# Kernel tuning notes

Hardware: AMD Instinct MI355X
Metric: run time of the kernel (lower is better)

The kernel has to match this reference:

```python
import jax, jax.numpy as jnp
import numpy as np
from jax import lax

B, C_IN, IMG, P = 8, 320, 64, 2
H = W = IMG // P            # 32
N = H * W                   # 1024 tokens
DIM = 128 * P * P           # 512
DEPTH, HEADS, DH = 6, 8, 64
INNER = HEADS * DH          # 512
MLP = 512
EPS = 1e-5


def layernorm(x, g, b):
    mu = x.mean(-1, keepdims=True)
    var = ((x - mu) ** 2).mean(-1, keepdims=True)
    return (x - mu) * lax.rsqrt(var + EPS) * g + b


def conv3x3(x, w, b):
    y = lax.conv_general_dilated(x, w, (1, 1), 'SAME',
                                 dimension_numbers=('NCHW', 'OIHW', 'NCHW'))
    return y + b[None, :, None, None]


def posemb_sincos_2d(h, w, dim, temperature=10000.0):
    y, x = jnp.meshgrid(jnp.arange(h, dtype=jnp.float32),
                        jnp.arange(w, dtype=jnp.float32), indexing='ij')
    omega = jnp.arange(dim // 4, dtype=jnp.float32) / (dim // 4 - 1)
    omega = 1.0 / (temperature ** omega)
    y = y.reshape(-1)[:, None] * omega[None, :]
    x = x.reshape(-1)[:, None] * omega[None, :]
    return jnp.concatenate([jnp.sin(x), jnp.cos(x), jnp.sin(y), jnp.cos(y)], axis=1)


def prepare_attn_mask(mask):
    # attn mask allows position pairs where either row or col token is marked.
    f = 64 // H
    m = (mask == 1)
    r = m.reshape(-1, H, f, W, f).any(axis=(2, 4)).reshape(-1, N)  # [M, N] bool
    return r[:, :, None] | r[:, None, :]                            # [M, N, N]


def setup_inputs() -> dict:
    key = jax.random.key(0)
    ks = jax.random.split(key, 24)
    s = 0.02
    d = dict(
        img=jax.random.normal(ks[0], (B, C_IN, IMG, IMG), jnp.float32),
        mask=jax.random.randint(ks[1], (DEPTH * B, 64, 64), 0, 2, jnp.int32),
        conv1_w=jax.random.normal(ks[2], (128, C_IN, 3, 3), jnp.float32) * s,
        conv1_b=jnp.zeros((128,), jnp.float32),
        ln_p_g=jnp.ones((DIM,), jnp.float32), ln_p_b=jnp.zeros((DIM,), jnp.float32),
        proj_w=jax.random.normal(ks[3], (DIM, DIM), jnp.float32) * s,
        proj_b=jnp.zeros((DIM,), jnp.float32),
        ln_q_g=jnp.ones((DIM,), jnp.float32), ln_q_b=jnp.zeros((DIM,), jnp.float32),
        attn_ln_g=jnp.ones((DEPTH, DIM), jnp.float32),
        attn_ln_b=jnp.zeros((DEPTH, DIM), jnp.float32),
        wqkv=jax.random.normal(ks[4], (DEPTH, DIM, 3 * INNER), jnp.float32) * s,
        wo=jax.random.normal(ks[5], (DEPTH, INNER, DIM), jnp.float32) * s,
        ff_ln_g=jnp.ones((DEPTH, DIM), jnp.float32),
        ff_ln_b=jnp.zeros((DEPTH, DIM), jnp.float32),
        w1=jax.random.normal(ks[6], (DEPTH, DIM, MLP), jnp.float32) * s,
        b1=jnp.zeros((DEPTH, MLP), jnp.float32),
        w2=jax.random.normal(ks[7], (DEPTH, MLP, DIM), jnp.float32) * s,
        b2=jnp.zeros((DEPTH, DIM), jnp.float32),
        conv2_w=jax.random.normal(ks[8], (C_IN, 128, 3, 3), jnp.float32) * s,
        conv2_b=jnp.zeros((C_IN,), jnp.float32),
    )
    return d


def reference(img, mask, conv1_w, conv1_b, ln_p_g, ln_p_b, proj_w, proj_b,
              ln_q_g, ln_q_b, attn_ln_g, attn_ln_b, wqkv, wo,
              ff_ln_g, ff_ln_b, w1, b1, w2, b2, conv2_w, conv2_b):
    am = prepare_attn_mask(mask).reshape(DEPTH, B, N, N)  # per-layer masks

    # patch embed: conv -> rearrange 'b c (h p1) (w p2) -> b (h w) (p1 p2 c)'
    y = conv3x3(img, conv1_w, conv1_b)                           # [B,128,64,64]
    y = y.reshape(B, 128, H, P, W, P).transpose(0, 2, 4, 3, 5, 1)
    y = y.reshape(B, N, P * P * 128)                             # [B,N,512]
    x = layernorm(y, ln_p_g, ln_p_b) @ proj_w + proj_b
    x = layernorm(x, ln_q_g, ln_q_b)
    x = x + posemb_sincos_2d(H, W, DIM).astype(x.dtype)

    scale = DH ** -0.5
    for i in range(DEPTH):
        xn = layernorm(x, attn_ln_g[i], attn_ln_b[i])
        qkv = xn @ wqkv[i]                                       # [B,N,3*INNER]
        q, k, v = jnp.split(qkv, 3, axis=-1)
        q, k, v = (t.reshape(B, N, HEADS, DH).transpose(0, 2, 1, 3)
                   for t in (q, k, v))
        dots = jnp.einsum('bhid,bhjd->bhij', q, k) * scale
        min_val = lax.stop_gradient(dots.min())
        dots = jnp.where(am[i][:, None, :, :], dots, min_val)
        attn = jax.nn.softmax(dots, axis=-1)
        o = jnp.einsum('bhij,bhjd->bhid', attn, v)
        o = o.transpose(0, 2, 1, 3).reshape(B, N, INNER) @ wo[i]
        x = o + x
        h = layernorm(x, ff_ln_g[i], ff_ln_b[i]) @ w1[i] + b1[i]
        x = jax.nn.gelu(h, approximate=False) @ w2[i] + b2[i] + x

    # 'b (h w) (p1 p2 c) -> b c (h p1) (w p2)' then conv
    z = x.reshape(B, H, W, P, P, 128).transpose(0, 5, 1, 3, 2, 4)
    z = z.reshape(B, 128, IMG, IMG)
    return conv3x3(z, conv2_w, conv2_b)
```

## Files before the change

kernel.cpp:

```cpp
#include <hip/hip_runtime.h>
#include <hip/hip_bf16.h>
#include <math.h>

typedef __attribute__((ext_vector_type(8))) short short8;
typedef __attribute__((ext_vector_type(4))) float f32x4;
typedef unsigned short u16;
typedef unsigned int u32;
typedef unsigned long long u64;

#define DEV __device__ __forceinline__

DEV float bf2f(u16 u){ u32 x = ((u32)u)<<16; return __builtin_bit_cast(float, x); }
DEV u16 f2bf(float f){ u32 x = __builtin_bit_cast(u32, f); return (u16)((x + 0x7FFFu + ((x>>16)&1u))>>16); }
DEV f32x4 mfma16(short8 a, short8 b, f32x4 c){ return __builtin_amdgcn_mfma_f32_16x16x32_bf16(a,b,c,0,0,0); }
DEV void gload16(const void* g, void* l){
  __builtin_amdgcn_global_load_lds((const __attribute__((address_space(1))) void*)g,
                                   (__attribute__((address_space(3))) void*)l, 16, 0, 0);
}
DEV u32 fkey(float f){ u32 b = __builtin_bit_cast(u32, f); return (b & 0x80000000u) ? ~b : (b ^ 0x80000000u); }
DEV float funkey(u32 k){ u32 b = (k & 0x80000000u) ? (k ^ 0x80000000u) : ~k; return __builtin_bit_cast(float, b); }
DEV u32 cvtpk(float lo, float hi){ u32 d; asm("v_cvt_pk_bf16_f32 %0, %1, %2" : "=v"(d) : "v"(lo), "v"(hi)); return d; }

static constexpr size_t O_PROJW = 0;
static constexpr size_t O_QKVW  = O_PROJW + 524288;
static constexpr size_t O_WOW   = O_QKVW + 9437184;
static constexpr size_t O_W1W   = O_WOW + 3145728;
static constexpr size_t O_W2W   = O_W1W + 3145728;
static constexpr size_t O_C1W   = O_W2W + 3145728;
static constexpr size_t O_C2W   = O_C1W + 737280;
static constexpr size_t O_RA    = O_C2W + 737280;
static constexpr size_t O_RB    = O_RA + 22302720;
static constexpr size_t O_X     = O_RB + 25165824;
static constexpr size_t O_D     = O_X + 16777216;
static constexpr size_t O_F     = O_D + 8388608;
static constexpr size_t O_RM    = O_F + 8388608;
static constexpr size_t O_MIN   = O_RM + 49152;
static constexpr size_t O_RMB   = O_MIN + 256;
static constexpr size_t WS_NEED = O_RMB + 8192;

__global__ __launch_bounds__(256) void k_transpose_bf(const float* __restrict__ src, u16* __restrict__ dst, int K, int N){
  __shared__ float tile[32][33];
  const int k0 = blockIdx.x*32, n0 = blockIdx.y*32;
  src += (size_t)blockIdx.z*K*N; dst += (size_t)blockIdx.z*K*N;
  const int c = threadIdx.x & 31, r4 = threadIdx.x >> 5;
  for(int r=r4; r<32; r+=8) tile[r][c] = src[(size_t)(k0+r)*N + n0+c];
  __syncthreads();
  for(int r=r4; r<32; r+=8) dst[(size_t)(n0+r)*K + k0+c] = f2bf(tile[c][r]);
}

__global__ __launch_bounds__(256) void k_convw(const float* __restrict__ src, u16* __restrict__ dst, int OC, int IC){
  int idx = blockIdx.x*256 + threadIdx.x;
  int total = OC*IC*9;
  if(idx >= total) return;
  int oc = idx/(IC*9); int rem = idx - oc*IC*9; int tap = rem/IC; int ic = rem - tap*IC;
  dst[idx] = f2bf(src[(size_t)(oc*IC+ic)*9 + tap]);
}

__global__ __launch_bounds__(256) void k_pad_img(const float* __restrict__ img, u16* __restrict__ pcl){
  const int by = blockIdx.x; const int b = by>>6, y = by&63; const int c0 = blockIdx.y*64;
  __shared__ float t[64][65];
  const int tx = threadIdx.x & 63, tz = threadIdx.x >> 6;
  for(int ci=tz; ci<64; ci+=4) t[ci][tx] = img[(((size_t)b*320 + c0+ci)*64 + y)*64 + tx];
  __syncthreads();
  for(int x=tz; x<64; x+=4) pcl[(((size_t)b*66 + y+1)*66 + (x+1))*320 + c0 + tx] = f2bf(t[tx][x]);
}

__global__ __launch_bounds__(256) void k_pad_tok(const float* __restrict__ x, u16* __restrict__ pcl){
  int idx = blockIdx.x*256 + threadIdx.x;
  const int c = idx & 127; int r = idx >> 7; const int xx = r & 63; r >>= 6; const int yy = r & 63; const int b = r >> 6;
  const int n = (yy>>1)*32 + (xx>>1); const int f = (yy&1)*256 + (xx&1)*128 + c;
  pcl[(((size_t)b*66 + yy+1)*66 + xx+1)*128 + c] = f2bf(x[((size_t)b*1024 + n)*512 + f]);
}

__global__ __launch_bounds__(256) void k_rmask(const int* __restrict__ mask, u64* __restrict__ rmbits){
  int idx = blockIdx.x*256 + threadIdx.x;
  const int m = idx >> 10, n = idx & 1023; const int h = n>>5, w = n&31;
  const int* mp = mask + ((size_t)m*64 + h*2)*64 + w*2;
  const int v = (mp[0]==1) | (mp[1]==1) | (mp[64]==1) | (mp[65]==1);
  const u64 bm = __ballot(v);
  if((threadIdx.x & 63) == 0) rmbits[idx>>6] = bm;
}

__global__ __launch_bounds__(256) void k_ln_bf(const float* __restrict__ in, const float* __restrict__ gw,
                                               const float* __restrict__ bw, u16* __restrict__ out){
  const int tok = blockIdx.x*4 + (threadIdx.x>>6);
  const int lane = threadIdx.x & 63;
  const float* rp = in + (size_t)tok*512 + lane*8;
  const float4 a = *(const float4*)rp;
  const float4 b = *(const float4*)(rp+4);
  float s  = a.x+a.y+a.z+a.w + b.x+b.y+b.z+b.w;
  float sq = a.x*a.x+a.y*a.y+a.z*a.z+a.w*a.w + b.x*b.x+b.y*b.y+b.z*b.z+b.w*b.w;
  #pragma unroll
  for(int off=1; off<64; off<<=1){ s += __shfl_xor(s,off); sq += __shfl_xor(sq,off); }
  const float mu = s*(1.f/512.f);
  const float rs = rsqrtf(fmaxf(sq*(1.f/512.f) - mu*mu, 0.f) + 1e-5f);
  const float4 g0 = *(const float4*)(gw + lane*8);
  const float4 g1 = *(const float4*)(gw + lane*8 + 4);
  const float4 b0 = *(const float4*)(bw + lane*8);
  const float4 b1 = *(const float4*)(bw + lane*8 + 4);
  short8 o8;
  o8[0]=f2bf((a.x-mu)*rs*g0.x+b0.x); o8[1]=f2bf((a.y-mu)*rs*g0.y+b0.y);
  o8[2]=f2bf((a.z-mu)*rs*g0.z+b0.z); o8[3]=f2bf((a.w-mu)*rs*g0.w+b0.w);
  o8[4]=f2bf((b.x-mu)*rs*g1.x+b1.x); o8[5]=f2bf((b.y-mu)*rs*g1.y+b1.y);
  o8[6]=f2bf((b.z-mu)*rs*g1.z+b1.z); o8[7]=f2bf((b.w-mu)*rs*g1.w+b1.w);
  *(short8*)(out + (size_t)tok*512 + lane*8) = o8;
}

__global__ __launch_bounds__(256) void k_lnq_pos(const float* __restrict__ in, const float* __restrict__ gw,
                                                 const float* __restrict__ bw, float* __restrict__ out){
  const int tok = blockIdx.x*4 + (threadIdx.x>>6);
  const int lane = threadIdx.x & 63;
  const float* rp = in + (size_t)tok*512 + lane*8;
  const float4 a = *(const float4*)rp;
  const float4 b = *(const float4*)(rp+4);
  float s  = a.x+a.y+a.z+a.w + b.x+b.y+b.z+b.w;
  float sq = a.x*a.x+a.y*a.y+a.z*a.z+a.w*a.w + b.x*b.x+b.y*b.y+b.z*b.z+b.w*b.w;
  #pragma unroll
  for(int off=1; off<64; off<<=1){ s += __shfl_xor(s,off); sq += __shfl_xor(sq,off); }
  const float mu = s*(1.f/512.f);
  const float rs = rsqrtf(fmaxf(sq*(1.f/512.f) - mu*mu, 0.f) + 1e-5f);
  const int n = tok & 1023; const int yy = n>>5, xx = n&31;
  const int f0 = lane*8; const int sec = f0>>7;
  const float coord = (sec<2) ? (float)xx : (float)yy;
  const float vv[8] = {a.x,a.y,a.z,a.w,b.x,b.y,b.z,b.w};
  float ov[8];
  #pragma unroll
  for(int j=0;j<8;j++){
    const int f = f0+j; const int qq = f & 127;
    const float om = __expf(-(float)qq * (9.2103403719761836f/127.f));
    const float arg = coord * om;
    const float pe = (sec&1) ? __cosf(arg) : __sinf(arg);
    ov[j] = (vv[j]-mu)*rs*gw[f] + bw[f] + pe;
  }
  float* op = out + (size_t)tok*512 + f0;
  *(float4*)op = (float4){ov[0],ov[1],ov[2],ov[3]};
  *(float4*)(op+4) = (float4){ov[4],ov[5],ov[6],ov[7]};
}

template<int EPI, int CONVC>
__global__ __launch_bounds__(256, 3)
void k_gemm(const u16* __restrict__ A, const u16* __restrict__ Wt,
            const float* __restrict__ bias, void* __restrict__ outp,
            const float* __restrict__ resid, int M, int N, int Kd)
{
  __shared__ u16 Ald[2][8192];
  __shared__ u16 Bld[2][4096];
  const int tid = threadIdx.x, lane = tid & 63, wv = tid >> 6;
  const int lr = lane & 15, g = lane >> 4;
  const int m0 = blockIdx.x * 128, n0 = blockIdx.y * 64;
  const int wm = wv * 32;
  const int srow = tid >> 3;
  const int sc  = (tid & 7) ^ (srow & 7);
  int b0=0, y0=0;
  if constexpr (CONVC != 0){ b0 = m0>>12; y0 = (m0>>6)&63; }
  const u16* ar[4];
  if constexpr (CONVC == 0){
    #pragma unroll
    for(int j=0;j<4;j++) ar[j] = A + (size_t)(m0+srow+32*j)*Kd + sc*8;
  }
  const u16* br0 = Wt + (size_t)(n0+srow)*Kd + sc*8;
  const u16* br1 = Wt + (size_t)(n0+srow+32)*Kd + sc*8;

  f32x4 acc[2][4];
  #pragma unroll
  for(int i=0;i<2;i++)
    #pragma unroll
    for(int j=0;j<4;j++) acc[i][j] = (f32x4){0.f,0.f,0.f,0.f};

  const int nIter = Kd >> 6;
  int cur = 0;

  auto stage = [&](int kt, int buf){
    const int k0 = kt << 6;
    if constexpr (CONVC != 0){
      const int tap = k0 / CONVC;
      const int ic0 = k0 - tap*CONVC;
      const int ky = tap/3, kx = tap - 3*(tap/3);
      #pragma unroll
      for(int j=0;j<4;j++){
        const int xr = srow + 32*(j&1);
        const int yr = y0 + (j>>1) + ky;
        const u16* ga = A + ((size_t)((b0*66 + yr)*66 + xr + kx))*CONVC + ic0 + sc*8;
        gload16(ga, &Ald[buf][j*2048 + tid*8]);
      }
    } else {
      #pragma unroll
      for(int j=0;j<4;j++) gload16(ar[j] + k0, &Ald[buf][j*2048 + tid*8]);
    }
    gload16(br0 + k0, &Bld[buf][tid*8]);
    gload16(br1 + k0, &Bld[buf][2048 + tid*8]);
  };

  stage(0, 0);
  for(int kt=0; kt<nIter; ++kt){
    __syncthreads();
    if(kt+1 < nIter) stage(kt+1, cur^1);
    short8 af[2][2], bg[4][2];
    #pragma unroll
    for(int mi=0;mi<2;mi++)
      #pragma unroll
      for(int kk=0;kk<2;kk++){
        const int R = wm + mi*16 + lr;
        const int c = kk*4 + g;
        af[mi][kk] = *(const short8*)&Ald[cur][R*64 + ((c ^ (R&7))<<3)];
      }
    #pragma unroll
    for(int nj=0;nj<4;nj++)
      #pragma unroll
      for(int kk=0;kk<2;kk++){
        const int Rn = nj*16 + lr;
        const int c = kk*4 + g;
        bg[nj][kk] = *(const short8*)&Bld[cur][Rn*64 + ((c ^ (Rn&7))<<3)];
      }
    #pragma unroll
    for(int mi=0;mi<2;mi++)
      #pragma unroll
      for(int nj=0;nj<4;nj++)
        #pragma unroll
        for(int kk=0;kk<2;kk++)
          acc[mi][nj] = mfma16(af[mi][kk], bg[nj][kk], acc[mi][nj]);
    cur ^= 1;
  }

  #pragma unroll
  for(int mi=0;mi<2;mi++){
    #pragma unroll
    for(int nj=0;nj<4;nj++){
      #pragma unroll
      for(int r=0;r<4;r++){
        const int mrow = m0 + wm + mi*16 + g*4 + r;
        const int ncol = n0 + nj*16 + lr;
        float val = acc[mi][nj][r];
        if constexpr (EPI==0 || EPI==3 || EPI==4 || EPI==5 || EPI==6)
          val += bias[ncol];
        if constexpr (EPI==0){
          ((float*)outp)[(size_t)mrow*512 + ncol] = val;
        } else if constexpr (EPI==2 || EPI==4){
          const size_t idx = (size_t)mrow*512 + ncol;
          ((float*)outp)[idx] = resid[idx] + val;
        } else if constexpr (EPI==3){
          const float gl = 0.5f * val * (1.f + erff(val * 0.70710678118654752f));
          ((u16*)outp)[(size_t)mrow*512 + ncol] = f2bf(gl);
        } else if constexpr (EPI==5){
          const int b = mrow>>12; const int rr = mrow&4095; const int y = rr>>6; const int xx = rr&63;
          const size_t pidx = ((size_t)(b*1024 + (y>>1)*32 + (xx>>1)))*512 + (y&1)*256 + (xx&1)*128 + ncol;
          ((float*)outp)[pidx] = val;
        } else if constexpr (EPI==6){
          const int b = mrow>>12; const int rr = mrow&4095; const int y = rr>>6; const int xx = rr&63;
          ((float*)outp)[(((size_t)(b*320 + ncol))*64 + y)*64 + xx] = val;
        }
      }
    }
  }
}

__global__ __launch_bounds__(256, 3)
void k_gemmW(const u16* __restrict__ A, const u16* __restrict__ Wt,
             void* __restrict__ outp, u16* __restrict__ vt, int Kd)
{
  __shared__ u16 Ald[2][8192];
  __shared__ u16 Bld[2][4096];
  const int tid = threadIdx.x, lane = tid & 63, wv = tid >> 6;
  const int lr = lane & 15, g = lane >> 4;
  const int m0 = blockIdx.x * 128, n0 = blockIdx.y * 64;
  const int wm = wv * 32;
  const int srow = tid >> 3;
  const int sc  = (tid & 7) ^ (srow & 7);
  const u16* ar[4];
  #pragma unroll
  for(int j=0;j<4;j++) ar[j] = A + (size_t)(m0+srow+32*j)*Kd + sc*8;
  const u16* br0 = Wt + (size_t)(n0+srow)*Kd + sc*8;
  const u16* br1 = Wt + (size_t)(n0+srow+32)*Kd + sc*8;

  f32x4 acc[2][4];
  #pragma unroll
  for(int i=0;i<2;i++)
    #pragma unroll
    for(int j=0;j<4;j++) acc[i][j] = (f32x4){0.f,0.f,0.f,0.f};

  const int nIter = Kd >> 6;
  int cur = 0;
  auto stage = [&](int kt, int buf){
    const int k0 = kt << 6;
    #pragma unroll
    for(int j=0;j<4;j++) gload16(ar[j] + k0, &Ald[buf][j*2048 + tid*8]);
    gload16(br0 + k0, &Bld[buf][tid*8]);
    gload16(br1 + k0, &Bld[buf][2048 + tid*8]);
  };

  stage(0, 0);
  for(int kt=0; kt<nIter; ++kt){
    __syncthreads();
    if(kt+1 < nIter) stage(kt+1, cur^1);
    short8 af[2][2], bg[4][2];
    #pragma unroll
    for(int mi=0;mi<2;mi++)
      #pragma unroll
      for(int kk=0;kk<2;kk++){
        const int R = wm + mi*16 + lr;
        const int c = kk*4 + g;
        af[mi][kk] = *(const short8*)&Ald[cur][R*64 + ((c ^ (R&7))<<3)];
      }
    #pragma unroll
    for(int nj=0;nj<4;nj++)
      #pragma unroll
      for(int kk=0;kk<2;kk++){
        const int Rn = nj*16 + lr;
        const int c = kk*4 + g;
        bg[nj][kk] = *(const short8*)&Bld[cur][Rn*64 + ((c ^ (Rn&7))<<3)];
      }
    #pragma unroll
    for(int mi=0;mi<2;mi++)
      #pragma unroll
      for(int nj=0;nj<4;nj++)
        #pragma unroll
        for(int kk=0;kk<2;kk++)
          acc[mi][nj] = mfma16(af[mi][kk], bg[nj][kk], acc[mi][nj]);
    cur ^= 1;
  }

  if(n0 < 1024){
    #pragma unroll
    for(int mi=0;mi<2;mi++){
      #pragma unroll
      for(int nj=0;nj<4;nj++){
        #pragma unroll
        for(int r=0;r<4;r++){
          const int mrow = m0 + wm + mi*16 + g*4 + r;
          const int ncol = n0 + nj*16 + lr;
          const int sec = ncol >> 9, rem = ncol & 511;
          const int head = rem >> 6, d = rem & 63;
          const int b = mrow >> 10, t = mrow & 1023;
          ((u16*)outp)[(size_t)sec*4194304 + ((size_t)((b*8+head)*1024 + t))*64 + d] = f2bf(acc[mi][nj][r]);
        }
      }
    }
  } else {
    const int head = (n0 - 1024) >> 6;
    const int b = m0 >> 10;
    const int t0 = m0 & 1023;
    const int bh = b*8 + head;
    __syncthreads();
    u16* Vt = (u16*)Ald;
    #pragma unroll
    for(int mi=0;mi<2;mi++)
      #pragma unroll
      for(int nj=0;nj<4;nj++)
        #pragma unroll
        for(int r=0;r<4;r++){
          const int lt = wm + mi*16 + g*4 + r;
          const int d  = nj*16 + lr;
          Vt[d*136 + lt] = f2bf(acc[mi][nj][r]);
        }
    __syncthreads();
    const int d = tid >> 2, qd = tid & 3;
    u16* dst = vt + (size_t)bh*65536 + (size_t)d*1024 + t0 + qd*32;
    const u16* srcl = &Vt[d*136 + qd*32];
    #pragma unroll
    for(int e4=0;e4<4;e4++)
      *(short8*)(dst + e4*8) = *(const short8*)(srcl + e4*8);
  }
}

__global__ __launch_bounds__(256, 4)
void k_attn_minmax(const u16* __restrict__ q, const u16* __restrict__ k, u32* __restrict__ keys, int layer){
  const int id = blockIdx.x;
  const int qt = (id>>3)&7;
  const int bh = ((id&7)<<3) | (id>>6);
  __shared__ u16 Kld[2][4096];
  __shared__ float redn[4], redx[4];
  const int tid = threadIdx.x, lane = tid & 63, wv = tid >> 6;
  const int lr = lane & 15, g = lane >> 4;
  const u16* qp0 = q + ((size_t)bh*1024 + qt*128 + wv*16 + lr)*64;
  const u16* qp1 = qp0 + 64*64;
  const short8 qa00 = *(const short8*)(qp0 + g*8);
  const short8 qa01 = *(const short8*)(qp0 + 32 + g*8);
  const short8 qa10 = *(const short8*)(qp1 + g*8);
  const short8 qa11 = *(const short8*)(qp1 + 32 + g*8);
  const u16* kbase = k + (size_t)bh*65536;
  const int srow = tid>>3, scs = lane&7;
  const int scg = scs ^ (srow&7);
  const int srow2 = srow + 32;
  const int scg2 = scs ^ (srow2&7);
  float mn = 3.0e38f, mx = -3.0e38f;
  gload16(kbase + (size_t)srow*64 + scg*8, &Kld[0][wv*512]);
  gload16(kbase + (size_t)srow2*64 + scg2*8, &Kld[0][2048 + wv*512]);
  int cur = 0;
  for(int jt=0; jt<16; ++jt){
    __syncthreads();
    if(jt < 15){
      const int j1 = (jt+1)*64;
      gload16(kbase + (size_t)(j1+srow)*64 + scg*8, &Kld[cur^1][wv*512]);
      gload16(kbase + (size_t)(j1+srow2)*64 + scg2*8, &Kld[cur^1][2048 + wv*512]);
    }
    #pragma unroll
    for(int c=0;c<4;c++){
      const int rr = c*16 + lr;
      const short8 kb0 = *(const short8*)&Kld[cur][rr*64 + ((g ^ (rr&7))<<3)];
      const short8 kb1 = *(const short8*)&Kld[cur][rr*64 + (((g+4) ^ (rr&7))<<3)];
      f32x4 sa = (f32x4){0.f,0.f,0.f,0.f};
      f32x4 sb = (f32x4){0.f,0.f,0.f,0.f};
      __builtin_amdgcn_s_setprio(1);
      sa = mfma16(qa00, kb0, sa);
      sa = mfma16(qa01, kb1, sa);
      sb = mfma16(qa10, kb0, sb);
      sb = mfma16(qa11, kb1, sb);
      __builtin_amdgcn_s_setprio(0);
      mn = fminf(mn, fminf(fminf(sa[0],sa[1]), fminf(sa[2],sa[3])));
      mx = fmaxf(mx, fmaxf(fmaxf(sa[0],sa[1]), fmaxf(sa[2],sa[3])));
      mn = fminf(mn, fminf(fminf(sb[0],sb[1]), fminf(sb[2],sb[3])));
      mx = fmaxf(mx, fmaxf(fmaxf(sb[0],sb[1]), fmaxf(sb[2],sb[3])));
    }
    cur ^= 1;
  }
  mn *= 0.125f; mx *= 0.125f;
  #pragma unroll
  for(int off=32; off; off>>=1){
    mn = fminf(mn, __shfl_down(mn, off));
    mx = fmaxf(mx, __shfl_down(mx, off));
  }
  if(lane==0){ redn[wv] = mn; redx[wv] = mx; }
  __syncthreads();
  if(tid==0){
    atomicMin(keys + layer,     fkey(fminf(fminf(redn[0],redn[1]), fminf(redn[2],redn[3]))));
    atomicMax(keys + 8 + layer, fkey(fmaxf(fmaxf(redx[0],redx[1]), fmaxf(redx[2],redx[3]))));
  }
}

__global__ __launch_bounds__(256, 3)
void k_attn(const u16* __restrict__ q, const u16* __restrict__ k, const u16* __restrict__ vt,
            const u64* __restrict__ rmbits, const u32* __restrict__ keys,
            u16* __restrict__ o, int layer){
  const int id = blockIdx.x;
  const int qt = (id>>3)&7;
  const int bh = ((id&7)<<3) | (id>>6);
  const int b = bh>>3, h = bh&7;
  __shared__ u16 Kld[2][4096];
  __shared__ u16 Vtld[2][4096];
  __shared__ u32 Pld[4][1024];
  const int tid = threadIdx.x, lane = tid & 63, wv = tid >> 6;
  const int lr = lane & 15, g = lane >> 4;
  const int L7 = lr & 7;
  const u16* qp0 = q + ((size_t)bh*1024 + qt*128 + wv*16 + lr)*64;
  const u16* qp1 = qp0 + 64*64;
  const short8 qa00 = *(const short8*)(qp0 + g*8);
  const short8 qa01 = *(const short8*)(qp0 + 32 + g*8);
  const short8 qa10 = *(const short8*)(qp1 + g*8);
  const short8 qa11 = *(const short8*)(qp1 + 32 + g*8);
  const float L2E = 1.44269504088896f;
  const float SC = 0.125f * L2E;
  float mnv = funkey(keys[layer]);
  float mxv = funkey(keys[8+layer]);
  if(!(mnv >= -1e38f && mnv <= 1e38f)) mnv = 0.f;
  if(!(mxv >= -1e38f && mxv <= 1e38f)) mxv = 0.f;
  const float ME   = mxv * L2E;
  const float minM = fmaxf(mnv*L2E - ME, -120.f);
  const u32* cbp = (const u32*)(rmbits + (size_t)(layer*8 + b)*16);
  const int rowi0 = qt*128 + wv*16 + lr;
  const int rowi1 = rowi0 + 64;
  const u32 rf0 = ((cbp[rowi0>>5] >> (rowi0&31)) & 1u) ? 0xFu : 0u;
  const u32 rf1 = ((cbp[rowi1>>5] >> (rowi1&31)) & 1u) ? 0xFu : 0u;
  u32* Pw = &Pld[wv][0];
  u32 wslot[4][2];
  #pragma unroll
  for(int c=0;c<4;c++){
    const int blk = c*2 + (g>>1);
    wslot[c][0] = lr*32 + ((blk ^ L7)<<2) + (g&1)*2;
    wslot[c][1] = wslot[c][0] + 1;
  }
  const u32 ra0 = lr*32 + ((g ^ L7)<<2);
  const u32 ra1 = lr*32 + (((4+g) ^ L7)<<2);

  float ls0 = 0.f, ls1 = 0.f;
  f32x4 acc0[4], acc1[4];
  #pragma unroll
  for(int d=0;d<4;d++){ acc0[d] = (f32x4){0.f,0.f,0.f,0.f}; acc1[d] = (f32x4){0.f,0.f,0.f,0.f}; }
  const u16* kbase = k + (size_t)bh*65536;
  const u16* vtbase = vt + (size_t)bh*65536;
  const int srow = tid>>3, scs = lane&7;
  const int scg = scs ^ (srow&7);
  const int srow2 = srow + 32;
  const int scg2 = scs ^ (srow2&7);
  gload16(kbase + (size_t)srow*64 + scg*8, &Kld[0][wv*512]);
  gload16(kbase + (size_t)srow2*64 + scg2*8, &Kld[0][2048 + wv*512]);
  gload16(vtbase + (size_t)srow*1024 + scg*8, &Vtld[0][wv*512]);
  gload16(vtbase + (size_t)srow2*1024 + scg2*8, &Vtld[0][2048 + wv*512]);
  int cur = 0;
  for(int jt=0; jt<16; ++jt){
    __syncthreads();
    if(jt < 15){
      const int j1 = (jt+1)*64;
      gload16(kbase + (size_t)(j1+srow)*64 + scg*8, &Kld[cur^1][wv*512]);
      gload16(kbase + (size_t)(j1+srow2)*64 + scg2*8, &Kld[cur^1][2048 + wv*512]);
      gload16(vtbase + (size_t)srow*1024 + j1 + scg*8, &Vtld[cur^1][wv*512]);
      gload16(vtbase + (size_t)srow2*1024 + j1 + scg2*8, &Vtld[cur^1][2048 + wv*512]);
    }
    const u32 cb_lo = cbp[jt*2], cb_hi = cbp[jt*2+1];
    #pragma unroll
    for(int c=0;c<4;c++){
      const int rr = c*16 + lr;
      const short8 kb0 = *(const short8*)&Kld[cur][rr*64 + ((g ^ (rr&7))<<3)];
      const short8 kb1 = *(const short8*)&Kld[cur][rr*64 + (((g+4) ^ (rr&7))<<3)];
      f32x4 sa = (f32x4){0.f,0.f,0.f,0.f};
      f32x4 sb = (f32x4){0.f,0.f,0.f,0.f};
      __builtin_amdgcn_s_setprio(1);
      sa = mfma16(kb0, qa00, sa);
      sa = mfma16(kb1, qa01, sa);
      sb = mfma16(kb0, qa10, sb);
      sb = mfma16(kb1, qa11, sb);
      __builtin_amdgcn_s_setprio(0);
      const u32 base = (((c<2) ? cb_lo : cb_hi) >> ((c&1)*16 + g*4));
      const u32 cw0 = base | rf0;
      const u32 cw1 = base | rf1;
      float e0[4], e1[4];
      #pragma unroll
      for(int r=0;r<4;r++){
        float sv0 = fmaxf(fmaf(sa[r], SC, -ME), -120.f);
        float sv1 = fmaxf(fmaf(sb[r], SC, -ME), -120.f);
        e0[r] = exp2f(((cw0 >> r) & 1u) ? sv0 : minM);
        e1[r] = exp2f(((cw1 >> r) & 1u) ? sv1 : minM);
        ls0 += e0[r]; ls1 += e1[r];
      }
      Pw[wslot[c][0]]       = cvtpk(e0[0], e0[1]);
      Pw[wslot[c][1]]       = cvtpk(e0[2], e0[3]);
      Pw[512 + wslot[c][0]] = cvtpk(e1[0], e1[1]);
      Pw[512 + wslot[c][1]] = cvtpk(e1[2], e1[3]);
    }
    asm volatile("s_waitcnt lgkmcnt(0)" ::: "memory");
    __builtin_amdgcn_sched_barrier(0);
    const short8 pa00 = *(const short8*)&Pw[ra0];
    const short8 pa01 = *(const short8*)&Pw[ra1];
    const short8 pa10 = *(const short8*)&Pw[512 + ra0];
    const short8 pa11 = *(const short8*)&Pw[512 + ra1];
    #pragma unroll
    for(int d=0;d<4;d++){
      const int rr = d*16 + lr;
      const short8 vb0 = *(const short8*)&Vtld[cur][rr*64 + ((g ^ (rr&7))<<3)];
      const short8 vb1 = *(const short8*)&Vtld[cur][rr*64 + (((g+4) ^ (rr&7))<<3)];
      __builtin_amdgcn_s_setprio(1);
      acc0[d] = mfma16(pa00, vb0, acc0[d]);
      acc0[d] = mfma16(pa01, vb1, acc0[d]);
      acc1[d] = mfma16(pa10, vb0, acc1[d]);
      acc1[d] = mfma16(pa11, vb1, acc1[d]);
      __builtin_amdgcn_s_setprio(0);
    }
    cur ^= 1;
  }
  ls0 += __shfl_xor(ls0, 16); ls0 += __shfl_xor(ls0, 32);
  ls1 += __shfl_xor(ls1, 16); ls1 += __shfl_xor(ls1, 32);
  float inv0[4], inv1[4];
  #pragma unroll
  for(int r=0;r<4;r++){ inv0[r] = 1.f / __shfl(ls0, g*4 + r); inv1[r] = 1.f / __shfl(ls1, g*4 + r); }
  #pragma unroll
  for(int d=0;d<4;d++)
    #pragma unroll
    for(int r=0;r<4;r++){
      const int qr0 = qt*128 + wv*16 + g*4 + r;
      o[((size_t)b*1024 + qr0)*512 + h*64 + d*16 + lr]        = f2bf(acc0[d][r] * inv0[r]);
      o[((size_t)b*1024 + qr0 + 64)*512 + h*64 + d*16 + lr]   = f2bf(acc1[d][r] * inv1[r]);
    }
}

extern "C" void kernel_launch(void* const* d_in, const int* in_sizes, int n_in,
                              void* d_out, int out_size, void* d_ws, size_t ws_size,
                              hipStream_t stream)
{
  const float* img     = (const float*)d_in[0];
  const int*   mask    = (const int*)d_in[1];
  const float* conv1_w = (const float*)d_in[2];
  const float* conv1_b = (const float*)d_in[3];
  const float* ln_p_g  = (const float*)d_in[4];
  const float* ln_p_b  = (const float*)d_in[5];
  const float* proj_w  = (const float*)d_in[6];
  const float* proj_b  = (const float*)d_in[7];
  const float* ln_q_g  = (const float*)d_in[8];
  const float* ln_q_b  = (const float*)d_in[9];
  const float* attn_ln_g = (const float*)d_in[10];
  const float* attn_ln_b = (const float*)d_in[11];
  const float* wqkv    = (const float*)d_in[12];
  const float* wo      = (const float*)d_in[13];
  const float* ff_ln_g = (const float*)d_in[14];
  const float* ff_ln_b = (const float*)d_in[15];
  const float* w1      = (const float*)d_in[16];
  const float* b1      = (const float*)d_in[17];
  const float* w2      = (const float*)d_in[18];
  const float* b2      = (const float*)d_in[19];
  const float* conv2_w = (const float*)d_in[20];
  const float* conv2_b = (const float*)d_in[21];

  if(ws_size < WS_NEED) return;
  char* ws = (char*)d_ws;
  u16* projWt = (u16*)(ws + O_PROJW);
  u16* qkvWt  = (u16*)(ws + O_QKVW);
  u16* woWt   = (u16*)(ws + O_WOW);
  u16* w1Wt   = (u16*)(ws + O_W1W);
  u16* w2Wt   = (u16*)(ws + O_W2W);
  u16* c1Wt   = (u16*)(ws + O_C1W);
  u16* c2Wt   = (u16*)(ws + O_C2W);
  u16* pcl    = (u16*)(ws + O_RA);
  float* tmpf = (float*)(ws + O_RA);
  u16* vtb    = (u16*)(ws + O_RA);
  float* patches = (float*)(ws + O_RB);
  u16* qkvb   = (u16*)(ws + O_RB);
  float* xbuf = (float*)(ws + O_X);
  u16* xnbf   = (u16*)(ws + O_D);
  u16* obf    = (u16*)(ws + O_F);
  u32* minbuf = (u32*)(ws + O_MIN);
  u64* rmbits = (u64*)(ws + O_RMB);

  hipMemsetAsync(ws + O_MIN, 0xFF, 32, stream);
  hipMemsetAsync(ws + O_MIN + 32, 0, 32, stream);
  hipMemsetAsync(ws + O_RA, 0, 22302720, stream);

  k_transpose_bf<<<dim3(16,16,1),256,0,stream>>>(proj_w, projWt, 512, 512);
  k_transpose_bf<<<dim3(16,48,6),256,0,stream>>>(wqkv,   qkvWt,  512, 1536);
  k_transpose_bf<<<dim3(16,16,6),256,0,stream>>>(wo,     woWt,   512, 512);
  k_transpose_bf<<<dim3(16,16,6),256,0,stream>>>(w1,     w1Wt,   512, 512);
  k_transpose_bf<<<dim3(16,16,6),256,0,stream>>>(w2,     w2Wt,   512, 512);
  k_convw<<<1440,256,0,stream>>>(conv1_w, c1Wt, 128, 320);
  k_convw<<<1440,256,0,stream>>>(conv2_w, c2Wt, 320, 128);
  k_rmask<<<192,256,0,stream>>>(mask, rmbits);

  k_pad_img<<<dim3(512,5),256,0,stream>>>(img, pcl);
  k_gemm<5,320><<<dim3(256,2),256,0,stream>>>(pcl, c1Wt, conv1_b, patches, nullptr, 32768, 128, 2880);
  k_ln_bf<<<2048,256,0,stream>>>(patches, ln_p_g, ln_p_b, xnbf);
  k_gemm<0,0><<<dim3(64,8),256,0,stream>>>(xnbf, projWt, proj_b, tmpf, nullptr, 8192, 512, 512);
  k_lnq_pos<<<2048,256,0,stream>>>(tmpf, ln_q_g, ln_q_b, xbuf);

  const u16* qb = qkvb;
  const u16* kb = qkvb + 4194304;
  for(int i=0;i<6;i++){
    k_ln_bf<<<2048,256,0,stream>>>(xbuf, attn_ln_g + i*512, attn_ln_b + i*512, xnbf);
    k_gemmW<<<dim3(64,24),256,0,stream>>>(xnbf, qkvWt + (size_t)i*1536*512, qkvb, vtb, 512);
    k_attn_minmax<<<512,256,0,stream>>>(qb, kb, minbuf, i);
    k_attn<<<512,256,0,stream>>>(qb, kb, vtb, rmbits, minbuf, obf, i);
    k_gemm<2,0><<<dim3(64,8),256,0,stream>>>(obf, woWt + (size_t)i*512*512, nullptr, xbuf, xbuf, 8192, 512, 512);
    k_ln_bf<<<2048,256,0,stream>>>(xbuf, ff_ln_g + i*512, ff_ln_b + i*512, xnbf);
    k_gemm<3,0><<<dim3(64,8),256,0,stream>>>(xnbf, w1Wt + (size_t)i*512*512, b1 + i*512, obf, nullptr, 8192, 512, 512);
    k_gemm<4,0><<<dim3(64,8),256,0,stream>>>(obf, w2Wt + (size_t)i*512*512, b2 + i*512, xbuf, xbuf, 8192, 512, 512);
  }

  hipMemsetAsync(ws + O_RA, 0, 8921088, stream);
  k_pad_tok<<<16384,256,0,stream>>>(xbuf, pcl);
  k_gemm<6,128><<<dim3(256,5),256,0,stream>>>(pcl, c2Wt, conv2_b, d_out, nullptr, 32768, 320, 1152);
}
```

Before: 975.6 us.

## Use 64x64 GEMM tiles, split minmax over key chunks, re-swizzle P LDS

```diff
diff --git a/kernel.cpp b/kernel.cpp
--- a/kernel.cpp
+++ b/kernel.cpp
@@ -135,6 +135,91 @@
   float* op = out + (size_t)tok*512 + f0;
   *(float4*)op = (float4){ov[0],ov[1],ov[2],ov[3]};
   *(float4*)(op+4) = (float4){ov[4],ov[5],ov[6],ov[7]};
+}
+
+template<int EPI>
+__global__ __launch_bounds__(256, 4)
+void k_gemm64(const u16* __restrict__ A, const u16* __restrict__ Wt,
+              const float* __restrict__ bias, void* __restrict__ outp,
+              const float* __restrict__ resid, int Kd)
+{
+  __shared__ u16 Ald[2][4096];
+  __shared__ u16 Bld[2][4096];
+  const int tid = threadIdx.x, lane = tid & 63, wv = tid >> 6;
+  const int lr = lane & 15, g = lane >> 4;
+  const int m0 = blockIdx.x * 64, n0 = blockIdx.y * 64;
+  const int wm = (wv >> 1) * 32, wn = (wv & 1) * 32;
+  const int srow = tid >> 3;
+  const int sc  = (tid & 7) ^ (srow & 7);
+  const u16* arow0p = A + (size_t)(m0+srow)*Kd + sc*8;
+  const u16* arow1p = A + (size_t)(m0+srow+32)*Kd + sc*8;
+  const u16* brow0p = Wt + (size_t)(n0+srow)*Kd + sc*8;
+  const u16* brow1p = Wt + (size_t)(n0+srow+32)*Kd + sc*8;
+
+  f32x4 acc[2][2];
+  #pragma unroll
+  for(int i=0;i<2;i++)
+    #pragma unroll
+    for(int j=0;j<2;j++) acc[i][j] = (f32x4){0.f,0.f,0.f,0.f};
+
+  const int nIter = Kd >> 6;
+  int cur = 0;
+  auto stage = [&](int kt, int buf){
+    const int k0 = kt << 6;
+    gload16(arow0p + k0, &Ald[buf][tid*8]);
+    gload16(arow1p + k0, &Ald[buf][2048 + tid*8]);
+    gload16(brow0p + k0, &Bld[buf][tid*8]);
+    gload16(brow1p + k0, &Bld[buf][2048 + tid*8]);
+  };
+
+  stage(0, 0);
+  for(int kt=0; kt<nIter; ++kt){
+    __syncthreads();
+    if(kt+1 < nIter) stage(kt+1, cur^1);
+    short8 af[2][2], bg[2][2];
+    #pragma unroll
+    for(int mi=0;mi<2;mi++)
+      #pragma unroll
+      for(int kk=0;kk<2;kk++){
+        const int R = wm + mi*16 + lr;
+        const int Rn = wn + mi*16 + lr;
+        const int c = kk*4 + g;
+        af[mi][kk] = *(const short8*)&Ald[cur][R*64 + ((c ^ (R&7))<<3)];
+        bg[mi][kk] = *(const short8*)&Bld[cur][Rn*64 + ((c ^ (Rn&7))<<3)];
+      }
+    #pragma unroll
+    for(int mi=0;mi<2;mi++)
+      #pragma unroll
+      for(int nj=0;nj<2;nj++)
+        #pragma unroll
+        for(int kk=0;kk<2;kk++)
+          acc[mi][nj] = mfma16(af[mi][kk], bg[nj][kk], acc[mi][nj]);
+    cur ^= 1;
+  }
+
+  #pragma unroll
+  for(int mi=0;mi<2;mi++){
+    #pragma unroll
+    for(int nj=0;nj<2;nj++){
+      #pragma unroll
+      for(int r=0;r<4;r++){
+        const int mrow = m0 + wm + mi*16 + g*4 + r;
+        const int ncol = n0 + wn + nj*16 + lr;
+        float val = acc[mi][nj][r];
+        if constexpr (EPI==0 || EPI==3 || EPI==4)
+          val += bias[ncol];
+        if constexpr (EPI==0){
+          ((float*)outp)[(size_t)mrow*512 + ncol] = val;
+        } else if constexpr (EPI==2 || EPI==4){
+          const size_t idx = (size_t)mrow*512 + ncol;
+          ((float*)outp)[idx] = resid[idx] + val;
+        } else if constexpr (EPI==3){
+          const float gl = 0.5f * val * (1.f + erff(val * 0.70710678118654752f));
+          ((u16*)outp)[(size_t)mrow*512 + ncol] = f2bf(gl);
+        }
+      }
+    }
+  }
 }
 
 template<int EPI, int CONVC>
@@ -230,18 +315,8 @@
       for(int r=0;r<4;r++){
         const int mrow = m0 + wm + mi*16 + g*4 + r;
         const int ncol = n0 + nj*16 + lr;
-        float val = acc[mi][nj][r];
-        if constexpr (EPI==0 || EPI==3 || EPI==4 || EPI==5 || EPI==6)
-          val += bias[ncol];
-        if constexpr (EPI==0){
-          ((float*)outp)[(size_t)mrow*512 + ncol] = val;
-        } else if constexpr (EPI==2 || EPI==4){
-          const size_t idx = (size_t)mrow*512 + ncol;
-          ((float*)outp)[idx] = resid[idx] + val;
-        } else if constexpr (EPI==3){
-          const float gl = 0.5f * val * (1.f + erff(val * 0.70710678118654752f));
-          ((u16*)outp)[(size_t)mrow*512 + ncol] = f2bf(gl);
-        } else if constexpr (EPI==5){
+        float val = acc[mi][nj][r] + bias[ncol];
+        if constexpr (EPI==5){
           const int b = mrow>>12; const int rr = mrow&4095; const int y = rr>>6; const int xx = rr&63;
           const size_t pidx = ((size_t)(b*1024 + (y>>1)*32 + (xx>>1)))*512 + (y&1)*256 + (xx&1)*128 + ncol;
           ((float*)outp)[pidx] = val;
@@ -365,8 +440,10 @@
 __global__ __launch_bounds__(256, 4)
 void k_attn_minmax(const u16* __restrict__ q, const u16* __restrict__ k, u32* __restrict__ keys, int layer){
   const int id = blockIdx.x;
-  const int qt = (id>>3)&7;
-  const int bh = ((id&7)<<3) | (id>>6);
+  const int t = id >> 3;
+  const int qt = t & 7;
+  const int js = (t >> 3) & 3;
+  const int bh = ((id & 7) << 3) | (t >> 5);
   __shared__ u16 Kld[2][4096];
   __shared__ float redn[4], redx[4];
   const int tid = threadIdx.x, lane = tid & 63, wv = tid >> 6;
@@ -383,16 +460,17 @@
   const int srow2 = srow + 32;
   const int scg2 = scs ^ (srow2&7);
   float mn = 3.0e38f, mx = -3.0e38f;
-  gload16(kbase + (size_t)srow*64 + scg*8, &Kld[0][wv*512]);
-  gload16(kbase + (size_t)srow2*64 + scg2*8, &Kld[0][2048 + wv*512]);
+  auto stageK = [&](int jt, int buf){
+    const int j0 = jt*64;
+    gload16(kbase + (size_t)(j0+srow)*64 + scg*8, &Kld[buf][wv*512]);
+    gload16(kbase + (size_t)(j0+srow2)*64 + scg2*8, &Kld[buf][2048 + wv*512]);
+  };
+  const int jt0 = js*4;
+  stageK(jt0, 0);
   int cur = 0;
-  for(int jt=0; jt<16; ++jt){
+  for(int i=0; i<4; ++i){
     __syncthreads();
-    if(jt < 15){
-      const int j1 = (jt+1)*64;
-      gload16(kbase + (size_t)(j1+srow)*64 + scg*8, &Kld[cur^1][wv*512]);
-      gload16(kbase + (size_t)(j1+srow2)*64 + scg2*8, &Kld[cur^1][2048 + wv*512]);
-    }
+    if(i < 3) stageK(jt0+i+1, cur^1);
     #pragma unroll
     for(int c=0;c<4;c++){
       const int rr = c*16 + lr;
@@ -441,6 +519,7 @@
   const int tid = threadIdx.x, lane = tid & 63, wv = tid >> 6;
   const int lr = lane & 15, g = lane >> 4;
   const int L7 = lr & 7;
+  const int LH = (lr >> 3) << 2;
   const u16* qp0 = q + ((size_t)bh*1024 + qt*128 + wv*16 + lr)*64;
   const u16* qp1 = qp0 + 64*64;
   const short8 qa00 = *(const short8*)(qp0 + g*8);
@@ -464,12 +543,12 @@
   u32 wslot[4][2];
   #pragma unroll
   for(int c=0;c<4;c++){
-    const int blk = c*2 + (g>>1);
-    wslot[c][0] = lr*32 + ((blk ^ L7)<<2) + (g&1)*2;
+    const int blk = (c*2 + (g>>1)) ^ L7 ^ LH;
+    wslot[c][0] = lr*32 + (blk<<2) + (g&1)*2;
     wslot[c][1] = wslot[c][0] + 1;
   }
-  const u32 ra0 = lr*32 + ((g ^ L7)<<2);
-  const u32 ra1 = lr*32 + (((4+g) ^ L7)<<2);
+  const u32 ra0 = lr*32 + ((g ^ L7 ^ LH)<<2);
+  const u32 ra1 = lr*32 + (((4+g) ^ L7 ^ LH)<<2);
 
   float ls0 = 0.f, ls1 = 0.f;
   f32x4 acc0[4], acc1[4];
@@ -624,7 +703,7 @@
   k_pad_img<<<dim3(512,5),256,0,stream>>>(img, pcl);
   k_gemm<5,320><<<dim3(256,2),256,0,stream>>>(pcl, c1Wt, conv1_b, patches, nullptr, 32768, 128, 2880);
   k_ln_bf<<<2048,256,0,stream>>>(patches, ln_p_g, ln_p_b, xnbf);
-  k_gemm<0,0><<<dim3(64,8),256,0,stream>>>(xnbf, projWt, proj_b, tmpf, nullptr, 8192, 512, 512);
+  k_gemm64<0><<<dim3(128,8),256,0,stream>>>(xnbf, projWt, proj_b, tmpf, nullptr, 512);
   k_lnq_pos<<<2048,256,0,stream>>>(tmpf, ln_q_g, ln_q_b, xbuf);
 
   const u16* qb = qkvb;
@@ -632,12 +711,12 @@
   for(int i=0;i<6;i++){
     k_ln_bf<<<2048,256,0,stream>>>(xbuf, attn_ln_g + i*512, attn_ln_b + i*512, xnbf);
     k_gemmW<<<dim3(64,24),256,0,stream>>>(xnbf, qkvWt + (size_t)i*1536*512, qkvb, vtb, 512);
-    k_attn_minmax<<<512,256,0,stream>>>(qb, kb, minbuf, i);
+    k_attn_minmax<<<2048,256,0,stream>>>(qb, kb, minbuf, i);
     k_attn<<<512,256,0,stream>>>(qb, kb, vtb, rmbits, minbuf, obf, i);
-    k_gemm<2,0><<<dim3(64,8),256,0,stream>>>(obf, woWt + (size_t)i*512*512, nullptr, xbuf, xbuf, 8192, 512, 512);
+    k_gemm64<2><<<dim3(128,8),256,0,stream>>>(obf, woWt + (size_t)i*512*512, nullptr, xbuf, xbuf, 512);
     k_ln_bf<<<2048,256,0,stream>>>(xbuf, ff_ln_g + i*512, ff_ln_b + i*512, xnbf);
-    k_gemm<3,0><<<dim3(64,8),256,0,stream>>>(xnbf, w1Wt + (size_t)i*512*512, b1 + i*512, obf, nullptr, 8192, 512, 512);
-    k_gemm<4,0><<<dim3(64,8),256,0,stream>>>(obf, w2Wt + (size_t)i*512*512, b2 + i*512, xbuf, xbuf, 8192, 512, 512);
+    k_gemm64<3><<<dim3(128,8),256,0,stream>>>(xnbf, w1Wt + (size_t)i*512*512, b1 + i*512, obf, nullptr, 512);
+    k_gemm64<4><<<dim3(128,8),256,0,stream>>>(obf, w2Wt + (size_t)i*512*512, b2 + i*512, xbuf, xbuf, 512);
   }
 
   hipMemsetAsync(ws + O_RA, 0, 8921088, stream);
```

Result: slower. 1.132 ms (+16.0%).
